# Kernel optimization log

Measured on AMD Instinct MI355X. Metric: run time of the kernel, lower is better.

The kernel has to match this reference:

```python
import jax, jax.numpy as jnp
import numpy as np

B, CIN, H, W = 8, 128, 64, 64
COUT, KH, KW = 128, 3, 3
STRIDE = (1, 1)
PAD = (1, 1)
DIL = (1, 1)
GROUPS = 1
OFFSET_GROUPS = 1

def _out_size(i, k, s, p, d):
    return (i + 2 * p - d * (k - 1) - 1) // s + 1

HO = _out_size(H, KH, STRIDE[0], PAD[0], DIL[0])
WO = _out_size(W, KW, STRIDE[1], PAD[1], DIL[1])


def setup_inputs() -> dict:
    key = jax.random.key(0)
    k1, k2, k3, k4 = jax.random.split(key, 4)
    x = jax.random.normal(k1, (B, CIN, H, W), jnp.float32)
    offset = jax.random.normal(k2, (B, 2 * OFFSET_GROUPS * KH * KW, HO, WO), jnp.float32)
    fan_in = (CIN // GROUPS) * KH * KW
    bound = 1.0 / np.sqrt(fan_in)
    weight = jax.random.uniform(k3, (COUT, CIN // GROUPS, KH, KW), jnp.float32, -bound, bound)
    bias = jax.random.uniform(k4, (COUT,), jnp.float32, -bound, bound)
    return {"x": x, "offset": offset, "weight": weight, "bias": bias}


def _deform_conv2d(x, offset, weight, bias):
    Bn, Cin, Hi, Wi = x.shape
    K = KH * KW
    Goff, Gw = OFFSET_GROUPS, GROUPS
    Cpg = Cin // Goff

    # base sampling positions (before learned offsets)
    ys = jnp.arange(HO, dtype=jnp.float32) * STRIDE[0] - PAD[0]  # [HO]
    xs = jnp.arange(WO, dtype=jnp.float32) * STRIDE[1] - PAD[1]  # [WO]
    base_y = jnp.repeat(jnp.arange(KH, dtype=jnp.float32) * DIL[0], KW)  # [K]
    base_x = jnp.tile(jnp.arange(KW, dtype=jnp.float32) * DIL[1], KH)    # [K]

    # offsets: channel layout is 2*(g*K + k) + {0: dy, 1: dx}
    off = offset.reshape(Bn, Goff, K, 2, HO, WO)
    py = base_y[None, None, :, None, None] + ys[None, None, None, :, None] + off[:, :, :, 0]  # [B,Goff,K,HO,WO]
    px = base_x[None, None, :, None, None] + xs[None, None, None, None, :] + off[:, :, :, 1]

    y0 = jnp.floor(py)
    x0 = jnp.floor(px)
    ly = py - y0  # fractional weights
    lx = px - x0

    xg = x.reshape(Bn, Goff, Cpg, Hi * Wi)

    def gather_one(img, lin):  # img [Cpg, H*W], lin [K,HO,WO] -> [Cpg,K,HO,WO]
        return img[:, lin]

    gather = jax.vmap(jax.vmap(gather_one))  # over B and Goff

    def corner(yi, xi, w):
        # zero-padding semantics: out-of-bounds corner contributes 0
        mask = (yi >= 0) & (yi < Hi) & (xi >= 0) & (xi < Wi)
        iy = jnp.clip(yi, 0, Hi - 1).astype(jnp.int32)
        ix = jnp.clip(xi, 0, Wi - 1).astype(jnp.int32)
        lin = iy * Wi + ix  # [B,Goff,K,HO,WO]
        wm = (w * mask.astype(x.dtype))[:, :, None]  # broadcast over channel axis
        return gather(xg, lin) * wm  # [B,Goff,Cpg,K,HO,WO]

    val = (corner(y0, x0, (1 - ly) * (1 - lx))
           + corner(y0, x0 + 1, (1 - ly) * lx)
           + corner(y0 + 1, x0, ly * (1 - lx))
           + corner(y0 + 1, x0 + 1, ly * lx))  # [B,Goff,Cpg,K,HO,WO]

    # grouped conv accumulate
    val = val.reshape(Bn, Gw, Cin // Gw, K, HO, WO)
    wg = weight.reshape(Gw, COUT // Gw, Cin // Gw, K)
    out = jnp.einsum('bgckhw,gock->bgohw', val, wg).reshape(Bn, COUT, HO, WO)
    return out + bias[None, :, None, None]


def reference(x, offset, weight, bias):
    return _deform_conv2d(x, offset, weight, bias)
```

## Files before the change

### kernel.cpp

```cpp
#include <hip/hip_runtime.h>

typedef unsigned int   u32;
typedef unsigned short u16;
typedef short bf16x8 __attribute__((ext_vector_type(8)));
typedef float f32x4  __attribute__((ext_vector_type(4)));
typedef float f32x2  __attribute__((ext_vector_type(2)));

#define CIN   128
#define COUT  128
#define Hh    64
#define Ww    64
#define Bb    8
#define NKSTEP 36
#define XT_ELEMS (Bb*Hh*Ww*CIN)

__device__ __forceinline__ float bflo(u32 u){ return __uint_as_float(u << 16); }
__device__ __forceinline__ float bfhi(u32 u){ return __uint_as_float(u & 0xffff0000u); }

__device__ __forceinline__ u32 pack2(float a, float b){
    u32 lo = __float_as_uint(a) + 0x8000u;
    u32 hi = __float_as_uint(b) + 0x8000u;
    return __builtin_amdgcn_perm(hi, lo, 0x07060302u);
}
__device__ __forceinline__ u16 tobf(float a){
    u32 ua = __float_as_uint(a);
    ua += 0x7fffu + ((ua >> 16) & 1u);
    return (u16)(ua >> 16);
}

__global__ __launch_bounds__(256) void k_transpose(const float* __restrict__ x,
                                                   u16* __restrict__ xT){
    __shared__ float lds[64*132];
    int bi = blockIdx.x;
    int hb = bi & 63, b = bi >> 6;
    int tid = threadIdx.x;

    {
        int r = tid >> 1, cq = tid & 1;
        const float* xp = x + ((size_t)(b*128 + r))*4096 + hb*64 + cq*32;
        float4 v[8];
#pragma unroll
        for (int k = 0; k < 8; ++k) v[k] = *(const float4*)(xp + k*4);
        float* dst = lds + (cq*32)*132 + r;
#pragma unroll
        for (int k = 0; k < 8; ++k){
            dst[(k*4+0)*132] = v[k].x;
            dst[(k*4+1)*132] = v[k].y;
            dst[(k*4+2)*132] = v[k].z;
            dst[(k*4+3)*132] = v[k].w;
        }
    }
    __syncthreads();
    {
        int s = tid >> 2, kq = tid & 3;
        const float* src = lds + s*132 + kq*32;
        u32 r16[16];
#pragma unroll
        for (int k = 0; k < 8; ++k){
            float4 v = *(const float4*)(src + k*4);
            r16[k*2  ] = pack2(v.x, v.y);
            r16[k*2+1] = pack2(v.z, v.w);
        }
        u32* dst = (u32*)xT + ((size_t)(b*4096 + hb*64 + s))*64 + kq*16;
#pragma unroll
        for (int k = 0; k < 4; ++k)
            *(uint4*)(dst + k*4) = *(uint4*)&r16[k*4];
    }
}

__global__ __launch_bounds__(256) void k_wprep(const float* __restrict__ w,
                                               u16* __restrict__ Wt){
    int gid = blockIdx.x*256 + threadIdx.x;
    int jf   = gid & 7;
    int lane = (gid >> 3) & 63;
    int mt   = (gid >> 9) & 7;
    int kt   = gid >> 12;
    int m  = mt*16 + (lane & 15);
    int kk = (lane >> 4)*8 + jf;
    int ck = kt*32 + kk;
    int kpos = ck >> 7;
    int cin  = ck & 127;
    Wt[gid] = tobf(w[((size_t)m*128 + cin)*9 + kpos]);
}

__global__ __launch_bounds__(256, 4)
void k_main(const float* __restrict__ off, const float* __restrict__ bias,
            const u16* __restrict__ xT, const u16* __restrict__ Wt,
            float* __restrict__ out){
    __shared__ u32 Vsm[2][32*20];

    int tid = threadIdx.x;
    int bi  = blockIdx.x;
    int b   = bi & 7;
    int t   = bi >> 3;
    int s0  = t * 32;
    int ho  = s0 >> 6, wo0 = s0 & 63;

    int p = tid >> 3, o = tid & 7;
    int wo = wo0 + p;
    const u16* xb = xT + (size_t)b * (Hh*Ww*CIN);
    const float* offp = off + ((size_t)b*18)*4096 + s0 + p;

    int lane = tid & 63, wave = tid >> 6;
    int wm = wave >> 1, wn = wave & 1;
    int quad = lane >> 4, l16 = lane & 15;

    f32x4 acc[4];
#pragma unroll
    for (int i = 0; i < 4; ++i) acc[i] = {0.f, 0.f, 0.f, 0.f};

    int   aaS[2][4];
    float wtS[2][4];
    float dyN, dxN;

    auto load_off = [&](int kpos){
        const float* op = offp + (size_t)(2*kpos)*4096;
        dyN = op[0];
        dxN = op[4096];
    };
    auto state = [&](int kpos, int st){
        float dy = dyN, dx = dxN;
        if (kpos < 8) load_off(kpos + 1);
        int kh = kpos / 3, kw = kpos - kh*3;
        float py = (float)(ho + kh - 1) + dy;
        float px = (float)(wo + kw - 1) + dx;
        float y0f = floorf(py), x0f = floorf(px);
        float ly = py - y0f, lx = px - x0f;
        int y0 = (int)y0f, x0 = (int)x0f;
        int y1 = y0 + 1,  x1 = x0 + 1;
        float my0 = (y0 >= 0 && y0 < Hh) ? 1.f : 0.f;
        float my1 = (y1 >= 0 && y1 < Hh) ? 1.f : 0.f;
        float mx0 = (x0 >= 0 && x0 < Ww) ? 1.f : 0.f;
        float mx1 = (x1 >= 0 && x1 < Ww) ? 1.f : 0.f;
        float oy = 1.f - ly, ox = 1.f - lx;
        wtS[st][0] = oy*ox*my0*mx0;
        wtS[st][1] = oy*lx*my0*mx1;
        wtS[st][2] = ly*ox*my1*mx0;
        wtS[st][3] = ly*lx*my1*mx1;
        int cy0 = min(max(y0,0),Hh-1), cy1 = min(max(y1,0),Hh-1);
        int cx0 = min(max(x0,0),Ww-1), cx1 = min(max(x1,0),Ww-1);
        aaS[st][0] = (cy0*Ww + cx0)*CIN;
        aaS[st][1] = (cy0*Ww + cx1)*CIN;
        aaS[st][2] = (cy1*Ww + cx0)*CIN;
        aaS[st][3] = (cy1*Ww + cx1)*CIN;
    };
    auto gather = [&](int c, uint2 q[4]){
        int st = (c >> 2) & 1;
        const u16* xc = xb + ((c & 3) << 5) + o*4;
#pragma unroll
        for (int cc = 0; cc < 4; ++cc)
            q[cc] = *(const uint2*)(xc + aaS[st][cc]);
    };
    auto loadA = [&](int c, uint4 a[4]){
        const u16* wp = Wt + (size_t)((c*8 + wm*4)*64 + lane)*8;
#pragma unroll
        for (int i = 0; i < 4; ++i)
            a[i] = *(const uint4*)(wp + (size_t)i*64*8);
    };
    auto blend_store = [&](const uint2 q[4], int st, int buf){
        u32 r2[2];
#pragma unroll
        for (int d = 0; d < 2; ++d){
            f32x2 s = {0.f, 0.f};
#pragma unroll
            for (int c = 0; c < 4; ++c){
                u32 u = ((const u32*)q)[c*2 + d];
                f32x2 v  = { bflo(u), bfhi(u) };
                f32x2 w2 = { wtS[st][c], wtS[st][c] };
                s += w2 * v;
            }
            r2[d] = pack2(s.x, s.y);
        }
        *(uint2*)&Vsm[buf][p*20 + o*2] = *(uint2*)&r2[0];
    };

    uint2 qb[2][4];
    uint4 av[2][4];
    load_off(0);
    state(0, 0);
    gather(0, qb[0]);
    loadA(0, av[0]);
    blend_store(qb[0], 0, 0);
    gather(1, qb[1]);

#pragma unroll
    for (int ks = 0; ks < NKSTEP; ++ks){
        __syncthreads();
        int c1 = ks + 1, c2 = ks + 2;
        if (c2 < NKSTEP){
            if ((c2 & 3) == 0) state(c2 >> 2, (c2 >> 2) & 1);
            gather(c2, qb[ks & 1]);
        }
        if (c1 < NKSTEP) loadA(c1, av[c1 & 1]);

        uint4 braw = *(const uint4*)&Vsm[ks & 1][(wn*16 + l16)*20 + quad*4];
        bf16x8 bv = __builtin_bit_cast(bf16x8, braw);
#pragma unroll
        for (int i = 0; i < 4; ++i){
            bf16x8 avv = __builtin_bit_cast(bf16x8, av[ks & 1][i]);
            acc[i] = __builtin_amdgcn_mfma_f32_16x16x32_bf16(avv, bv, acc[i], 0, 0, 0);
        }

        if (c1 < NKSTEP)
            blend_store(qb[c1 & 1], (c1 >> 2) & 1, c1 & 1);
    }

    int pcol = wn*16 + l16;
#pragma unroll
    for (int i = 0; i < 4; ++i){
        int cout0 = (wm*4 + i)*16 + quad*4;
        size_t obase = ((size_t)(b*COUT + cout0))*4096 + (s0 + pcol);
#pragma unroll
        for (int r = 0; r < 4; ++r)
            out[obase + (size_t)r*4096] = acc[i][r] + bias[cout0 + r];
    }
}

extern "C" void kernel_launch(void* const* d_in, const int* in_sizes, int n_in,
                              void* d_out, int out_size, void* d_ws, size_t ws_size,
                              hipStream_t stream){
    const float* x    = (const float*)d_in[0];
    const float* off  = (const float*)d_in[1];
    const float* w    = (const float*)d_in[2];
    const float* bias = (const float*)d_in[3];
    float* out = (float*)d_out;

    u16* xT = (u16*)d_ws;
    u16* Wt = xT + XT_ELEMS;

    k_transpose<<<dim3(512),  dim3(256), 0, stream>>>(x, xT);
    k_wprep    <<<dim3(576),  dim3(256), 0, stream>>>(w, Wt);
    k_main     <<<dim3(1024), dim3(256), 0, stream>>>(off, bias, xT, Wt, out);
}
```

Baseline: 118.3 us.

## Double pixel tile to a full row and gather whole kernel position per stage

Each block now handles one full output row of 64 pixels instead of 32. Each thread gathers all 128 channels' bilinear corners for a kernel position in one stage with 16-byte loads, and the LDS buffer holds four K-chunks. This reuses each weight A-fragment across two MFMA column tiles and cuts synchronisation from 36 barriers to 9. In exchange it uses far more registers (a 64-entry uint4 ring plus doubled accumulators), lowers launch bounds to 2 blocks per SM, and halves the grid to 512 blocks, which may reduce occupancy and latency hiding.

```diff
diff --git a/kernel.cpp b/kernel.cpp
--- a/kernel.cpp
+++ b/kernel.cpp
@@ -11,7 +11,7 @@
 #define Hh    64
 #define Ww    64
 #define Bb    8
-#define NKSTEP 36
+#define NKPOS 9
 #define XT_ELEMS (Bb*Hh*Ww*CIN)
 
 __device__ __forceinline__ float bflo(u32 u){ return __uint_as_float(u << 16); }
@@ -83,21 +83,17 @@
     Wt[gid] = tobf(w[((size_t)m*128 + cin)*9 + kpos]);
 }
 
-__global__ __launch_bounds__(256, 4)
+__global__ __launch_bounds__(256, 2)
 void k_main(const float* __restrict__ off, const float* __restrict__ bias,
             const u16* __restrict__ xT, const u16* __restrict__ Wt,
             float* __restrict__ out){
-    __shared__ u32 Vsm[2][32*20];
-
-    int tid = threadIdx.x;
-    int bi  = blockIdx.x;
-    int b   = bi & 7;
-    int t   = bi >> 3;
-    int s0  = t * 32;
-    int ho  = s0 >> 6, wo0 = s0 & 63;
-
-    int p = tid >> 3, o = tid & 7;
-    int wo = wo0 + p;
+    __shared__ u32 Vsm[2][4*64*20];
+
+    int tid = threadIdx.x, bi = blockIdx.x;
+    int b = bi & 7, t = bi >> 3;
+    int s0 = t * 64;
+
+    int p = tid >> 2, qt = tid & 3;
     const u16* xb = xT + (size_t)b * (Hh*Ww*CIN);
     const float* offp = off + ((size_t)b*18)*4096 + s0 + p;
 
@@ -105,13 +101,17 @@
     int wm = wave >> 1, wn = wave & 1;
     int quad = lane >> 4, l16 = lane & 15;
 
-    f32x4 acc[4];
-#pragma unroll
-    for (int i = 0; i < 4; ++i) acc[i] = {0.f, 0.f, 0.f, 0.f};
+    f32x4 acc[4][2];
+#pragma unroll
+    for (int i = 0; i < 4; ++i)
+#pragma unroll
+        for (int j = 0; j < 2; ++j) acc[i][j] = {0.f,0.f,0.f,0.f};
 
     int   aaS[2][4];
     float wtS[2][4];
     float dyN, dxN;
+    uint4 ring[4][4];
+    uint4 av[2][4];
 
     auto load_off = [&](int kpos){
         const float* op = offp + (size_t)(2*kpos)*4096;
@@ -120,10 +120,9 @@
     };
     auto state = [&](int kpos, int st){
         float dy = dyN, dx = dxN;
-        if (kpos < 8) load_off(kpos + 1);
         int kh = kpos / 3, kw = kpos - kh*3;
-        float py = (float)(ho + kh - 1) + dy;
-        float px = (float)(wo + kw - 1) + dx;
+        float py = (float)(t + kh - 1) + dy;
+        float px = (float)(p + kw - 1) + dx;
         float y0f = floorf(py), x0f = floorf(px);
         float ly = py - y0f, lx = px - x0f;
         int y0 = (int)y0f, x0 = (int)x0f;
@@ -144,75 +143,92 @@
         aaS[st][2] = (cy1*Ww + cx0)*CIN;
         aaS[st][3] = (cy1*Ww + cx1)*CIN;
     };
-    auto gather = [&](int c, uint2 q[4]){
-        int st = (c >> 2) & 1;
-        const u16* xc = xb + ((c & 3) << 5) + o*4;
-#pragma unroll
-        for (int cc = 0; cc < 4; ++cc)
-            q[cc] = *(const uint2*)(xc + aaS[st][cc]);
-    };
-    auto loadA = [&](int c, uint4 a[4]){
-        const u16* wp = Wt + (size_t)((c*8 + wm*4)*64 + lane)*8;
+    auto gather = [&](int st){
+#pragma unroll
+        for (int c = 0; c < 4; ++c){
+            const u16* xc = xb + aaS[st][c] + qt*32;
+#pragma unroll
+            for (int s = 0; s < 4; ++s)
+                ring[c][s] = *(const uint4*)(xc + s*8);
+        }
+    };
+    auto loadA = [&](int gc, uint4 a[4]){
+        const u16* wp = Wt + (size_t)((gc*8 + wm*4)*64 + lane)*8;
 #pragma unroll
         for (int i = 0; i < 4; ++i)
             a[i] = *(const uint4*)(wp + (size_t)i*64*8);
     };
-    auto blend_store = [&](const uint2 q[4], int st, int buf){
-        u32 r2[2];
-#pragma unroll
-        for (int d = 0; d < 2; ++d){
-            f32x2 s = {0.f, 0.f};
-#pragma unroll
-            for (int c = 0; c < 4; ++c){
-                u32 u = ((const u32*)q)[c*2 + d];
-                f32x2 v  = { bflo(u), bfhi(u) };
-                f32x2 w2 = { wtS[st][c], wtS[st][c] };
-                s += w2 * v;
+    auto blend_store = [&](int st, int buf){
+        u32* dst = &Vsm[buf][qt*1280 + p*20];
+#pragma unroll
+        for (int s = 0; s < 4; ++s){
+            u32 r4[4];
+#pragma unroll
+            for (int d = 0; d < 4; ++d){
+                f32x2 s2 = {0.f, 0.f};
+#pragma unroll
+                for (int c = 0; c < 4; ++c){
+                    u32 u = ((const u32*)&ring[c][s])[d];
+                    f32x2 v  = { bflo(u), bfhi(u) };
+                    f32x2 w2 = { wtS[st][c], wtS[st][c] };
+                    s2 += w2 * v;
+                }
+                r4[d] = pack2(s2.x, s2.y);
             }
-            r2[d] = pack2(s.x, s.y);
-        }
-        *(uint2*)&Vsm[buf][p*20 + o*2] = *(uint2*)&r2[0];
-    };
-
-    uint2 qb[2][4];
-    uint4 av[2][4];
+            *(uint2*)(dst + s*4    ) = *(uint2*)&r4[0];
+            *(uint2*)(dst + s*4 + 2) = *(uint2*)&r4[2];
+        }
+    };
+
     load_off(0);
     state(0, 0);
-    gather(0, qb[0]);
+    gather(0);
+    load_off(1);
+    state(1, 1);
+    blend_store(0, 0);
     loadA(0, av[0]);
-    blend_store(qb[0], 0, 0);
-    gather(1, qb[1]);
-
-#pragma unroll
-    for (int ks = 0; ks < NKSTEP; ++ks){
+
+#pragma unroll
+    for (int g = 0; g < NKPOS; ++g){
         __syncthreads();
-        int c1 = ks + 1, c2 = ks + 2;
-        if (c2 < NKSTEP){
-            if ((c2 & 3) == 0) state(c2 >> 2, (c2 >> 2) & 1);
-            gather(c2, qb[ks & 1]);
-        }
-        if (c1 < NKSTEP) loadA(c1, av[c1 & 1]);
-
-        uint4 braw = *(const uint4*)&Vsm[ks & 1][(wn*16 + l16)*20 + quad*4];
-        bf16x8 bv = __builtin_bit_cast(bf16x8, braw);
-#pragma unroll
-        for (int i = 0; i < 4; ++i){
-            bf16x8 avv = __builtin_bit_cast(bf16x8, av[ks & 1][i]);
-            acc[i] = __builtin_amdgcn_mfma_f32_16x16x32_bf16(avv, bv, acc[i], 0, 0, 0);
-        }
-
-        if (c1 < NKSTEP)
-            blend_store(qb[c1 & 1], (c1 >> 2) & 1, c1 & 1);
-    }
-
-    int pcol = wn*16 + l16;
+        if (g + 1 < NKPOS) gather((g + 1) & 1);
+        if (g + 2 < NKPOS) load_off(g + 2);
+
+#pragma unroll
+        for (int c = 0; c < 4; ++c){
+            int gc = g*4 + c;
+            if (gc + 1 < 4*NKPOS) loadA(gc + 1, av[(gc + 1) & 1]);
+
+            uint4 braw[2];
+#pragma unroll
+            for (int j = 0; j < 2; ++j)
+                braw[j] = *(const uint4*)&Vsm[g & 1][c*1280 + ((wn*2 + j)*16 + l16)*20 + quad*4];
+#pragma unroll
+            for (int i = 0; i < 4; ++i){
+                bf16x8 avv = __builtin_bit_cast(bf16x8, av[gc & 1][i]);
+#pragma unroll
+                for (int j = 0; j < 2; ++j){
+                    bf16x8 bv = __builtin_bit_cast(bf16x8, braw[j]);
+                    acc[i][j] = __builtin_amdgcn_mfma_f32_16x16x32_bf16(avv, bv, acc[i][j], 0, 0, 0);
+                }
+            }
+        }
+
+        if (g + 2 < NKPOS) state(g + 2, g & 1);
+        if (g + 1 < NKPOS) blend_store((g + 1) & 1, (g + 1) & 1);
+    }
+
 #pragma unroll
     for (int i = 0; i < 4; ++i){
         int cout0 = (wm*4 + i)*16 + quad*4;
-        size_t obase = ((size_t)(b*COUT + cout0))*4096 + (s0 + pcol);
-#pragma unroll
-        for (int r = 0; r < 4; ++r)
-            out[obase + (size_t)r*4096] = acc[i][r] + bias[cout0 + r];
+#pragma unroll
+        for (int j = 0; j < 2; ++j){
+            int pcol = (wn*2 + j)*16 + l16;
+            size_t obase = ((size_t)(b*COUT + cout0))*4096 + (s0 + pcol);
+#pragma unroll
+            for (int r = 0; r < 4; ++r)
+                out[obase + (size_t)r*4096] = acc[i][j][r] + bias[cout0 + r];
+        }
     }
 }
 
@@ -228,7 +244,7 @@
     u16* xT = (u16*)d_ws;
     u16* Wt = xT + XT_ELEMS;
 
-    k_transpose<<<dim3(512),  dim3(256), 0, stream>>>(x, xT);
-    k_wprep    <<<dim3(576),  dim3(256), 0, stream>>>(w, Wt);
-    k_main     <<<dim3(1024), dim3(256), 0, stream>>>(off, bias, xT, Wt, out);
-}
+    k_transpose<<<dim3(512), dim3(256), 0, stream>>>(x, xT);
+    k_wprep    <<<dim3(576), dim3(256), 0, stream>>>(w, Wt);
+    k_main     <<<dim3(512), dim3(256), 0, stream>>>(off, bias, xT, Wt, out);
+}
```

Measured after the change: 113.0 us. -4.5%, faster.
